# Optimization experiments

Hardware: AMD Instinct MI355X
Metric: run time of the kernel (lower is better)

## Reference

```python
import jax, jax.numpy as jnp
import numpy as np

DIM = 2048
NUM_HEADS = 16
HEAD_DIM = DIM // NUM_HEADS
ROPE_BASE = 10000.0


def _rotate_half(t):
    t1, t2 = jnp.split(t, 2, axis=-1)
    return jnp.concatenate([-t2, t1], axis=-1)


def _rope_sin_cos(seq_len):
    # fp32 angles, matching RoPE1D
    inv_freq = 1.0 / (ROPE_BASE ** (jnp.arange(0, HEAD_DIM, 2, dtype=jnp.float32) / HEAD_DIM))
    freqs = jnp.arange(seq_len, dtype=jnp.float32)[:, None] * inv_freq[None, :]  # [S, hd/2]
    angles = jnp.concatenate([freqs, freqs], axis=-1)  # [S, hd]
    return jnp.sin(angles), jnp.cos(angles)


def setup_inputs() -> dict:
    key = jax.random.key(0)
    ks = jax.random.split(key, 5)
    B, S = 2, 2048
    x = jax.random.normal(ks[0], (B, S, DIM), dtype=jnp.float32)
    scale = 1.0 / np.sqrt(DIM)
    W_qkv = jax.random.normal(ks[1], (DIM, 3 * DIM), dtype=jnp.float32) * scale
    b_qkv = jnp.zeros((3 * DIM,), dtype=jnp.float32)
    W_proj = jax.random.normal(ks[2], (DIM, DIM), dtype=jnp.float32) * scale
    b_proj = jnp.zeros((DIM,), dtype=jnp.float32)
    return {"x": x, "W_qkv": W_qkv, "b_qkv": b_qkv, "W_proj": W_proj, "b_proj": b_proj}


def reference(x, W_qkv, b_qkv, W_proj, b_proj):
    B, S, D = x.shape
    H, hd = NUM_HEADS, HEAD_DIM
    qkv = x @ W_qkv + b_qkv  # [B, S, 3D]
    qkv = qkv.reshape(B, S, 3, H, hd)
    q, k, v = qkv[:, :, 0], qkv[:, :, 1], qkv[:, :, 2]  # [B, S, H, hd]
    q, k, v = (t.transpose(0, 2, 1, 3) for t in (q, k, v))  # [B, H, S, hd]
    sin, cos = _rope_sin_cos(S)  # [S, hd]
    sin = sin[None, None]
    cos = cos[None, None]
    q = q * cos + _rotate_half(q) * sin
    k = k * cos + _rotate_half(k) * sin
    # scaled dot-product attention (non-causal, no mask, no dropout)
    scale = 1.0 / np.sqrt(hd).astype(np.float32)
    scores = jnp.einsum("bhqd,bhkd->bhqk", q, k) * scale
    attn = jax.nn.softmax(scores, axis=-1)
    out = jnp.einsum("bhqk,bhkd->bhqd", attn, v)  # [B, H, S, hd]
    out = out.transpose(0, 2, 1, 3).reshape(B, S, D)
    return out @ W_proj + b_proj
```

## Files before the change

### kernel.cpp

```cpp
#include <hip/hip_runtime.h>


typedef __attribute__((ext_vector_type(4))) float  f32x4;
typedef __attribute__((ext_vector_type(8))) short  short8;
typedef __attribute__((ext_vector_type(4))) float  fv4;
typedef __attribute__((ext_vector_type(4))) unsigned short us4;

#define MFMA16(accv, av, bv) \
  asm volatile("v_mfma_f32_16x16x32_bf16 %0, %1, %2, %0" : "+v"(accv) : "v"(av), "v"(bv))

__device__ __forceinline__ unsigned short f2bf(float f) {
  unsigned int u = __float_as_uint(f);
  u += 0x7fffu + ((u >> 16) & 1u);
  return (unsigned short)(u >> 16);
}

__device__ __forceinline__ void gl_lds16(const void* g, void* l) {
  __builtin_amdgcn_global_load_lds((const __attribute__((address_space(1))) void*)g,
                                   (__attribute__((address_space(3))) void*)l, 16, 0, 0);
}

__global__ void cvt_f32_bf16(const float* __restrict__ in,
                             unsigned short* __restrict__ out, int n4) {
  int i = blockIdx.x * blockDim.x + threadIdx.x;
  int stride = gridDim.x * blockDim.x;
  for (; i < n4; i += stride) {
    fv4 v = ((const fv4*)in)[i];
    us4 o;
    o[0] = f2bf(v[0]); o[1] = f2bf(v[1]); o[2] = f2bf(v[2]); o[3] = f2bf(v[3]);
    ((us4*)out)[i] = o;
  }
}

__global__ void transpose_cvt(const float* __restrict__ in,
                              unsigned short* __restrict__ out, int R, int C) {
  __shared__ float tile[32][33];
  int c0 = blockIdx.x * 32, r0 = blockIdx.y * 32;
  int tx = threadIdx.x, ty = threadIdx.y;
#pragma unroll
  for (int i = 0; i < 4; i++)
    tile[ty + i * 8][tx] = in[(size_t)(r0 + ty + i * 8) * C + c0 + tx];
  __syncthreads();
#pragma unroll
  for (int i = 0; i < 4; i++)
    out[(size_t)(c0 + ty + i * 8) * R + r0 + tx] = f2bf(tile[tx][ty + i * 8]);
}

__global__ __launch_bounds__(256, 2) void qkv_gemm(
    const unsigned short* __restrict__ A,
    const unsigned short* __restrict__ Bt,
    const float* __restrict__ bias,
    unsigned short* __restrict__ Qo,
    unsigned short* __restrict__ Ko,
    unsigned short* __restrict__ Vo)
{
  __shared__ __align__(16) unsigned short Al[128 * 64];
  __shared__ __align__(16) unsigned short Bl[128 * 64];

  const int NBX = 48, NWG = 1536;
  int bid = blockIdx.x;
  int nid = (bid & 7) * (NWG / 8) + (bid >> 3);
  int by = nid / NBX, bx = nid - by * NBX;

  int tid = threadIdx.x;
  int wv = tid >> 6, lane = tid & 63;
  int wr = wv >> 1, wc = wv & 1;
  int g = lane >> 4, c = lane & 15;

  int m0 = by * 128, n0 = bx * 128;

  f32x4 acc[4][4];
#pragma unroll
  for (int m = 0; m < 4; m++)
#pragma unroll
    for (int n = 0; n < 4; n++)
#pragma unroll
      for (int r = 0; r < 4; r++) acc[m][n][r] = 0.f;

  for (int k0 = 0; k0 < 2048; k0 += 64) {
#pragma unroll
    for (int i = 0; i < 4; i++) {
      int s = wv * 256 + i * 64 + lane;
      int row = s >> 3;
      int cb = (s & 7) ^ (row & 7);
      gl_lds16(A  + (size_t)(m0 + row) * 2048 + k0 + cb * 8,
               Al + (size_t)(wv * 256 + i * 64) * 8);
      gl_lds16(Bt + (size_t)(n0 + row) * 2048 + k0 + cb * 8,
               Bl + (size_t)(wv * 256 + i * 64) * 8);
    }
    __syncthreads();

    short8 af[4][2], bf[4][2];
#pragma unroll
    for (int m = 0; m < 4; m++) {
      int row = wr * 64 + m * 16 + c;
#pragma unroll
      for (int kc = 0; kc < 2; kc++)
        af[m][kc] = *(const short8*)(Al + row * 64 + (((kc * 4 + g) ^ (row & 7)) * 8));
    }
#pragma unroll
    for (int n = 0; n < 4; n++) {
      int gt = 2 * wc + (n & 1) + (n >> 1) * 4;
      int row = gt * 16 + c;
#pragma unroll
      for (int kc = 0; kc < 2; kc++)
        bf[n][kc] = *(const short8*)(Bl + row * 64 + (((kc * 4 + g) ^ (row & 7)) * 8));
    }
#pragma unroll
    for (int m = 0; m < 4; m++)
#pragma unroll
      for (int n = 0; n < 4; n++) {
        MFMA16(acc[m][n], af[m][0], bf[n][0]);
        MFMA16(acc[m][n], af[m][1], bf[n][1]);
      }
    __syncthreads();
  }

  int sel = bx >> 4;
  int h = bx & 15;
  int b = by >> 4;

  int dloc[4];
  float biasv[4];
#pragma unroll
  for (int n = 0; n < 4; n++) {
    int gt = 2 * wc + (n & 1) + (n >> 1) * 4;
    dloc[n] = gt * 16 + c;
    biasv[n] = bias[n0 + dloc[n]];
  }

  if (sel == 2) {
    unsigned short* Vs = Al;
    for (int p = 0; p < 2; p++) {
      if (wr == p) {
#pragma unroll
        for (int m = 0; m < 4; m++)
#pragma unroll
          for (int n = 0; n < 4; n++) {
            int d = dloc[n];
#pragma unroll
            for (int r = 0; r < 4; r++) {
              int srel = m * 16 + 4 * g + r;
              Vs[d * 64 + (srel ^ ((d & 7) << 3))] = f2bf(acc[m][n][r] + biasv[n]);
            }
          }
      }
      __syncthreads();
#pragma unroll
      for (int i = 0; i < 4; i++) {
        int seg = i * 256 + tid;
        int d = seg >> 3, slot = seg & 7;
        short8 val = *(const short8*)(Vs + d * 64 + ((slot ^ (d & 7)) * 8));
        int s_seq = (by & 15) * 128 + p * 64 + slot * 8;
        *(short8*)(Vo + ((size_t)((b * 16 + h) * 128 + d)) * 2048 + s_seq) = val;
      }
      __syncthreads();
    }
  } else {
    unsigned short* outp = (sel == 0) ? Qo : Ko;
    float qscale = (sel == 0) ? (0.08838834764831845f * 1.44269504088896340736f) : 1.0f;
    float invf[2];
#pragma unroll
    for (int j = 0; j < 2; j++)
      invf[j] = __expf(-(float)dloc[j] * 0.14391156831212787f);
    int srow_base = (by & 15) * 128 + wr * 64;
#pragma unroll
    for (int m = 0; m < 4; m++) {
#pragma unroll
      for (int j = 0; j < 2; j++) {
        int dlo = dloc[j];
#pragma unroll
        for (int r = 0; r < 4; r++) {
          int s_seq = srow_base + m * 16 + 4 * g + r;
          float ang = (float)s_seq * invf[j];
          float sn, cs;
          __sincosf(ang, &sn, &cs);
          float vlo = acc[m][j][r]     + biasv[j];
          float vhi = acc[m][j + 2][r] + biasv[j + 2];
          float rlo = (vlo * cs - vhi * sn) * qscale;
          float rhi = (vhi * cs + vlo * sn) * qscale;
          size_t base = ((size_t)((b * 16 + h) * 2048 + s_seq)) * 128;
          outp[base + dlo]      = f2bf(rlo);
          outp[base + dlo + 64] = f2bf(rhi);
        }
      }
    }
  }
}

__global__ __launch_bounds__(256, 2) void attn_kernel(
    const unsigned short* __restrict__ Qi,
    const unsigned short* __restrict__ Ki,
    const unsigned short* __restrict__ Vi,
    unsigned short* __restrict__ X2)
{
  __shared__ __align__(16) unsigned short Kl[2][64 * 128];
  __shared__ __align__(16) unsigned short Vl[2][128 * 64];
  __shared__ __align__(16) unsigned short Pl[4][32 * 64];

  int bid = blockIdx.x;
  int nid = (bid & 7) * 64 + (bid >> 3);
  int bh = nid >> 4, qblk = nid & 15;
  int tid = threadIdx.x, wv = tid >> 6, lane = tid & 63;
  int g = lane >> 4, c = lane & 15;

  const unsigned short* Kg = Ki + (size_t)bh * 2048 * 128;
  const unsigned short* Vg = Vi + (size_t)bh * 128 * 2048;
  const unsigned short* Qb = Qi + ((size_t)bh * 2048 + qblk * 128 + wv * 32) * 128;

  short8 qf[2][4];
#pragma unroll
  for (int qt = 0; qt < 2; qt++)
#pragma unroll
    for (int dc = 0; dc < 4; dc++)
      qf[qt][dc] = *(const short8*)(Qb + (size_t)(qt * 16 + c) * 128 + dc * 32 + g * 8);

  f32x4 accO[2][8];
#pragma unroll
  for (int qt = 0; qt < 2; qt++)
#pragma unroll
    for (int nt = 0; nt < 8; nt++)
#pragma unroll
      for (int r = 0; r < 4; r++) accO[qt][nt][r] = 0.f;
  float m_run[2] = {-3.0e38f, -3.0e38f};
  float l_run[2] = {0.f, 0.f};

  auto stage = [&](int bsel, int t0) {
#pragma unroll
    for (int j = 0; j < 4; j++) {
      int e = j * 256 + tid;
      int s = e >> 4, sl = e & 15;
      gl_lds16(Kg + (size_t)(t0 + s) * 128 + ((sl ^ (s & 7)) * 8),
               &Kl[bsel][(size_t)(j * 256 + wv * 64) * 8]);
    }
#pragma unroll
    for (int j = 0; j < 4; j++) {
      int e = j * 256 + tid;
      int d = e >> 3, sl = e & 7;
      gl_lds16(Vg + (size_t)d * 2048 + t0 + ((sl ^ (d & 7)) * 8),
               &Vl[bsel][(size_t)(j * 256 + wv * 64) * 8]);
    }
  };

  stage(0, 0);
  __syncthreads();

  int cur = 0;
  for (int t = 0; t < 32; t++) {
    if (t < 31) stage(cur ^ 1, (t + 1) * 64);

    const unsigned short* Kt_ = &Kl[cur][0];
    const unsigned short* Vt_ = &Vl[cur][0];
    unsigned short* Pw = &Pl[wv][0];

    f32x4 sc[2][4];
#pragma unroll
    for (int qt = 0; qt < 2; qt++)
#pragma unroll
      for (int kt = 0; kt < 4; kt++)
#pragma unroll
        for (int r = 0; r < 4; r++) sc[qt][kt][r] = 0.f;

#pragma unroll
    for (int kt = 0; kt < 4; kt++) {
      short8 kf[4];
#pragma unroll
      for (int dc = 0; dc < 4; dc++)
        kf[dc] = *(const short8*)(Kt_ + (size_t)(kt * 16 + c) * 128 +
                                  (((dc * 4 + g) ^ (c & 7)) * 8));
      __builtin_amdgcn_s_setprio(1);
#pragma unroll
      for (int dc = 0; dc < 4; dc++) {
        MFMA16(sc[0][kt], kf[dc], qf[0][dc]);
        MFMA16(sc[1][kt], kf[dc], qf[1][dc]);
      }
      __builtin_amdgcn_s_setprio(0);
    }

    float mx[2];
#pragma unroll
    for (int qt = 0; qt < 2; qt++) {
      f32x4 mv = sc[qt][0];
#pragma unroll
      for (int kt = 1; kt < 4; kt++)
#pragma unroll
        for (int r = 0; r < 4; r++) mv[r] = fmaxf(mv[r], sc[qt][kt][r]);
      float m0 = fmaxf(fmaxf(mv[0], mv[1]), fmaxf(mv[2], mv[3]));
      m0 = fmaxf(m0, __shfl_xor(m0, 16));
      m0 = fmaxf(m0, __shfl_xor(m0, 32));
      mx[qt] = m0;
    }
    if (__any((mx[0] > m_run[0]) || (mx[1] > m_run[1]))) {
#pragma unroll
      for (int qt = 0; qt < 2; qt++) {
        float mnew = fmaxf(m_run[qt], mx[qt]);
        float al = __builtin_exp2f(m_run[qt] - mnew);
        l_run[qt] *= al;
        m_run[qt] = mnew;
#pragma unroll
        for (int r = 0; r < 4; r++) {
          float alr = __shfl(al, 4 * g + r);
#pragma unroll
          for (int nt = 0; nt < 8; nt++) accO[qt][nt][r] *= alr;
        }
      }
    }
#pragma unroll
    for (int qt = 0; qt < 2; qt++) {
      float rs = 0.f;
#pragma unroll
      for (int kt = 0; kt < 4; kt++) {
        float p0 = __builtin_exp2f(sc[qt][kt][0] - m_run[qt]);
        float p1 = __builtin_exp2f(sc[qt][kt][1] - m_run[qt]);
        float p2 = __builtin_exp2f(sc[qt][kt][2] - m_run[qt]);
        float p3 = __builtin_exp2f(sc[qt][kt][3] - m_run[qt]);
        rs += (p0 + p1) + (p2 + p3);
        unsigned int lo, hi;
        asm("v_cvt_pk_bf16_f32 %0, %1, %2" : "=v"(lo) : "v"(p0), "v"(p1));
        asm("v_cvt_pk_bf16_f32 %0, %1, %2" : "=v"(hi) : "v"(p2), "v"(p3));
        uint2 pk; pk.x = lo; pk.y = hi;
        *(uint2*)(Pw + (size_t)(qt * 16 + c) * 64 +
                  (((kt * 2 + (g >> 1)) ^ (c & 7)) * 8) + (g & 1) * 4) = pk;
      }
      rs += __shfl_xor(rs, 16);
      rs += __shfl_xor(rs, 32);
      l_run[qt] += rs;
    }

    short8 pa[2][2];
#pragma unroll
    for (int qt = 0; qt < 2; qt++)
#pragma unroll
      for (int kc = 0; kc < 2; kc++)
        pa[qt][kc] = *(const short8*)(Pw + (size_t)(qt * 16 + c) * 64 +
                                      (((kc * 4 + g) ^ (c & 7)) * 8));
#pragma unroll
    for (int nt = 0; nt < 8; nt++) {
      short8 vf0 = *(const short8*)(Vt_ + (size_t)(nt * 16 + c) * 64 +
                                    ((g ^ (c & 7)) * 8));
      short8 vf1 = *(const short8*)(Vt_ + (size_t)(nt * 16 + c) * 64 +
                                    (((4 + g) ^ (c & 7)) * 8));
      __builtin_amdgcn_s_setprio(1);
      MFMA16(accO[0][nt], pa[0][0], vf0);
      MFMA16(accO[1][nt], pa[1][0], vf0);
      MFMA16(accO[0][nt], pa[0][1], vf1);
      MFMA16(accO[1][nt], pa[1][1], vf1);
      __builtin_amdgcn_s_setprio(0);
    }

    __syncthreads();
    cur ^= 1;
  }

  float rl[2] = {1.f / l_run[0], 1.f / l_run[1]};
  int b = bh >> 4, h = bh & 15;
  size_t rowbase = (size_t)b * 2048 + qblk * 128 + wv * 32;
#pragma unroll
  for (int qt = 0; qt < 2; qt++)
#pragma unroll
    for (int r = 0; r < 4; r++) {
      float rr = __shfl(rl[qt], 4 * g + r);
      size_t row = rowbase + qt * 16 + 4 * g + r;
#pragma unroll
      for (int nt = 0; nt < 8; nt++)
        X2[row * 2048 + h * 128 + nt * 16 + c] = f2bf(accO[qt][nt][r] * rr);
    }
}

__global__ __launch_bounds__(256, 2) void proj_gemm(
    const unsigned short* __restrict__ A,
    const unsigned short* __restrict__ Bt,
    const float* __restrict__ bias,
    float* __restrict__ Co)
{
  __shared__ __align__(16) unsigned short Al[128 * 64];
  __shared__ __align__(16) unsigned short Bl[128 * 64];

  const int NBX = 16, NWG = 512;
  int bid = blockIdx.x;
  int nid = (bid & 7) * (NWG / 8) + (bid >> 3);
  int by = nid / NBX, bx = nid - by * NBX;

  int tid = threadIdx.x;
  int wv = tid >> 6, lane = tid & 63;
  int wr = wv >> 1, wc = wv & 1;
  int g = lane >> 4, c = lane & 15;

  int m0 = by * 128, n0 = bx * 128;

  f32x4 acc[4][4];
#pragma unroll
  for (int m = 0; m < 4; m++)
#pragma unroll
    for (int n = 0; n < 4; n++)
#pragma unroll
      for (int r = 0; r < 4; r++) acc[m][n][r] = 0.f;

  for (int k0 = 0; k0 < 2048; k0 += 64) {
#pragma unroll
    for (int i = 0; i < 4; i++) {
      int s = wv * 256 + i * 64 + lane;
      int row = s >> 3;
      int cb = (s & 7) ^ (row & 7);
      gl_lds16(A  + (size_t)(m0 + row) * 2048 + k0 + cb * 8,
               Al + (size_t)(wv * 256 + i * 64) * 8);
      gl_lds16(Bt + (size_t)(n0 + row) * 2048 + k0 + cb * 8,
               Bl + (size_t)(wv * 256 + i * 64) * 8);
    }
    __syncthreads();

    short8 af[4][2], bf[4][2];
#pragma unroll
    for (int m = 0; m < 4; m++) {
      int row = wr * 64 + m * 16 + c;
#pragma unroll
      for (int kc = 0; kc < 2; kc++)
        af[m][kc] = *(const short8*)(Al + row * 64 + (((kc * 4 + g) ^ (row & 7)) * 8));
    }
#pragma unroll
    for (int n = 0; n < 4; n++) {
      int row = wc * 64 + n * 16 + c;
#pragma unroll
      for (int kc = 0; kc < 2; kc++)
        bf[n][kc] = *(const short8*)(Bl + row * 64 + (((kc * 4 + g) ^ (row & 7)) * 8));
    }
#pragma unroll
    for (int m = 0; m < 4; m++)
#pragma unroll
      for (int n = 0; n < 4; n++) {
        MFMA16(acc[m][n], af[m][0], bf[n][0]);
        MFMA16(acc[m][n], af[m][1], bf[n][1]);
      }
    __syncthreads();
  }

#pragma unroll
  for (int m = 0; m < 4; m++)
#pragma unroll
    for (int n = 0; n < 4; n++)
#pragma unroll
      for (int r = 0; r < 4; r++) {
        int row = m0 + wr * 64 + m * 16 + 4 * g + r;
        int col = n0 + wc * 64 + n * 16 + c;
        Co[(size_t)row * 2048 + col] = acc[m][n][r] + bias[col];
      }
}

extern "C" void kernel_launch(void* const* d_in, const int* in_sizes, int n_in,
                              void* d_out, int out_size, void* d_ws, size_t ws_size,
                              hipStream_t stream) {
  (void)in_sizes; (void)n_in; (void)out_size; (void)ws_size;

  const float* x      = (const float*)d_in[0];
  const float* W_qkv  = (const float*)d_in[1];
  const float* b_qkv  = (const float*)d_in[2];
  const float* W_proj = (const float*)d_in[3];
  const float* b_proj = (const float*)d_in[4];
  float* out = (float*)d_out;

  unsigned short* xb     = (unsigned short*)d_ws;
  unsigned short* wqkvT  = xb     + 8388608;
  unsigned short* wprojT = wqkvT  + 12582912;
  unsigned short* Qb     = wprojT + 4194304;
  unsigned short* Kb     = Qb     + 8388608;
  unsigned short* Vtb    = Kb     + 8388608;
  unsigned short* x2     = Vtb    + 8388608;

  cvt_f32_bf16<<<2048, 256, 0, stream>>>(x, xb, 8388608 / 4);
  transpose_cvt<<<dim3(192, 64), dim3(32, 8), 0, stream>>>(W_qkv, wqkvT, 2048, 6144);
  transpose_cvt<<<dim3(64, 64),  dim3(32, 8), 0, stream>>>(W_proj, wprojT, 2048, 2048);
  qkv_gemm<<<1536, 256, 0, stream>>>(xb, wqkvT, b_qkv, Qb, Kb, Vtb);
  attn_kernel<<<512, 256, 0, stream>>>(Qb, Kb, Vtb, x2);
  proj_gemm<<<512, 256, 0, stream>>>(x2, wprojT, b_proj, out);
}
```

Baseline: 397.6 us.

## Enlarge GEMM tiles and add 4-stage async LDS pipeline with waitcnt-based sync

```diff
diff --git a/kernel.cpp b/kernel.cpp
--- a/kernel.cpp
+++ b/kernel.cpp
@@ -46,7 +46,7 @@
     out[(size_t)(c0 + ty + i * 8) * R + r0 + tx] = f2bf(tile[tx][ty + i * 8]);
 }
 
-__global__ __launch_bounds__(256, 2) void qkv_gemm(
+__global__ __launch_bounds__(512, 2) void qkv_gemm(
     const unsigned short* __restrict__ A,
     const unsigned short* __restrict__ Bt,
     const float* __restrict__ bias,
@@ -54,124 +54,130 @@
     unsigned short* __restrict__ Ko,
     unsigned short* __restrict__ Vo)
 {
-  __shared__ __align__(16) unsigned short Al[128 * 64];
-  __shared__ __align__(16) unsigned short Bl[128 * 64];
-
-  const int NBX = 48, NWG = 1536;
+  __shared__ __align__(16) unsigned short SH[65536];
+
+  const int NWG = 384;
   int bid = blockIdx.x;
   int nid = (bid & 7) * (NWG / 8) + (bid >> 3);
-  int by = nid / NBX, bx = nid - by * NBX;
+  int by = nid / 24, bx = nid - by * 24;
 
   int tid = threadIdx.x;
   int wv = tid >> 6, lane = tid & 63;
-  int wr = wv >> 1, wc = wv & 1;
+  int wr = wv >> 2, wc = wv & 3;
   int g = lane >> 4, c = lane & 15;
 
-  int m0 = by * 128, n0 = bx * 128;
-
-  f32x4 acc[4][4];
-#pragma unroll
-  for (int m = 0; m < 4; m++)
+  int m0 = by * 256, n0 = bx * 256;
+
+  int lh = wc >> 1, jj = wc & 1;
+  int F[4];
+#pragma unroll
+  for (int n = 0; n < 4; n++) F[n] = 8 * lh + 2 * jj + (n & 1) + ((n >> 1) << 2);
+
+  f32x4 acc[8][4];
+#pragma unroll
+  for (int m = 0; m < 8; m++)
 #pragma unroll
     for (int n = 0; n < 4; n++)
 #pragma unroll
       for (int r = 0; r < 4; r++) acc[m][n][r] = 0.f;
 
-  for (int k0 = 0; k0 < 2048; k0 += 64) {
-#pragma unroll
-    for (int i = 0; i < 4; i++) {
-      int s = wv * 256 + i * 64 + lane;
-      int row = s >> 3;
-      int cb = (s & 7) ^ (row & 7);
-      gl_lds16(A  + (size_t)(m0 + row) * 2048 + k0 + cb * 8,
-               Al + (size_t)(wv * 256 + i * 64) * 8);
-      gl_lds16(Bt + (size_t)(n0 + row) * 2048 + k0 + cb * 8,
-               Bl + (size_t)(wv * 256 + i * 64) * 8);
-    }
+  auto stage = [&](int buf, int kt) {
+    int k0 = kt * 32;
+    unsigned short* Ad = SH + buf * 8192;
+    unsigned short* Bd = SH + 32768 + buf * 8192;
+#pragma unroll
+    for (int p = 0; p < 2; p++) {
+      int e = p * 512 + tid;
+      int row = e >> 2, sl = (e & 3) ^ ((row >> 1) & 3);
+      gl_lds16(A  + (size_t)(m0 + row) * 2048 + k0 + sl * 8,
+               Ad + p * 4096 + wv * 512);
+      gl_lds16(Bt + (size_t)(n0 + row) * 2048 + k0 + sl * 8,
+               Bd + p * 4096 + wv * 512);
+    }
+  };
+
+  stage(0, 0); stage(1, 1); stage(2, 2);
+
+  for (int t = 0; t < 64; t++) {
+    if (t < 62)       asm volatile("s_waitcnt vmcnt(8)" ::: "memory");
+    else if (t == 62) asm volatile("s_waitcnt vmcnt(4)" ::: "memory");
+    else              asm volatile("s_waitcnt vmcnt(0)" ::: "memory");
+    __builtin_amdgcn_s_barrier();
+
+    const unsigned short* Ab = SH + (t & 3) * 8192;
+    const unsigned short* Bb = SH + 32768 + (t & 3) * 8192;
+
+    short8 af[8], bfv[4];
+#pragma unroll
+    for (int m = 0; m < 8; m++) {
+      int row = wr * 128 + m * 16 + c;
+      af[m] = *(const short8*)(Ab + row * 32 + ((g ^ ((row >> 1) & 3)) << 3));
+    }
+#pragma unroll
+    for (int n = 0; n < 4; n++) {
+      int row = F[n] * 16 + c;
+      bfv[n] = *(const short8*)(Bb + row * 32 + ((g ^ ((row >> 1) & 3)) << 3));
+    }
+
+    if (t < 61) stage((t + 3) & 3, t + 3);
+
+    __builtin_amdgcn_s_setprio(1);
+#pragma unroll
+    for (int m = 0; m < 8; m++)
+#pragma unroll
+      for (int n = 0; n < 4; n++)
+        MFMA16(acc[m][n], af[m], bfv[n]);
+    __builtin_amdgcn_s_setprio(0);
+  }
+
+  int sel = bx >> 3;
+  int bxl = bx & 7;
+  int b = by >> 3;
+
+  float biasv[4];
+#pragma unroll
+  for (int n = 0; n < 4; n++) biasv[n] = bias[n0 + F[n] * 16 + c];
+
+  if (sel == 2) {
     __syncthreads();
-
-    short8 af[4][2], bf[4][2];
-#pragma unroll
-    for (int m = 0; m < 4; m++) {
-      int row = wr * 64 + m * 16 + c;
-#pragma unroll
-      for (int kc = 0; kc < 2; kc++)
-        af[m][kc] = *(const short8*)(Al + row * 64 + (((kc * 4 + g) ^ (row & 7)) * 8));
-    }
-#pragma unroll
-    for (int n = 0; n < 4; n++) {
-      int gt = 2 * wc + (n & 1) + (n >> 1) * 4;
-      int row = gt * 16 + c;
-#pragma unroll
-      for (int kc = 0; kc < 2; kc++)
-        bf[n][kc] = *(const short8*)(Bl + row * 64 + (((kc * 4 + g) ^ (row & 7)) * 8));
-    }
-#pragma unroll
-    for (int m = 0; m < 4; m++)
+    unsigned short* Vs = SH;
+#pragma unroll
+    for (int m = 0; m < 8; m++)
 #pragma unroll
       for (int n = 0; n < 4; n++) {
-        MFMA16(acc[m][n], af[m][0], bf[n][0]);
-        MFMA16(acc[m][n], af[m][1], bf[n][1]);
+        int dp = F[n] * 16 + c;
+        int sb = wr * 128 + m * 16 + 4 * g;
+        us4 pk;
+#pragma unroll
+        for (int r = 0; r < 4; r++) pk[r] = f2bf(acc[m][n][r] + biasv[n]);
+        *(us4*)(Vs + dp * 256 + (sb ^ ((dp & 7) << 3))) = pk;
       }
     __syncthreads();
-  }
-
-  int sel = bx >> 4;
-  int h = bx & 15;
-  int b = by >> 4;
-
-  int dloc[4];
-  float biasv[4];
-#pragma unroll
-  for (int n = 0; n < 4; n++) {
-    int gt = 2 * wc + (n & 1) + (n >> 1) * 4;
-    dloc[n] = gt * 16 + c;
-    biasv[n] = bias[n0 + dloc[n]];
-  }
-
-  if (sel == 2) {
-    unsigned short* Vs = Al;
-    for (int p = 0; p < 2; p++) {
-      if (wr == p) {
-#pragma unroll
-        for (int m = 0; m < 4; m++)
-#pragma unroll
-          for (int n = 0; n < 4; n++) {
-            int d = dloc[n];
-#pragma unroll
-            for (int r = 0; r < 4; r++) {
-              int srel = m * 16 + 4 * g + r;
-              Vs[d * 64 + (srel ^ ((d & 7) << 3))] = f2bf(acc[m][n][r] + biasv[n]);
-            }
-          }
-      }
-      __syncthreads();
-#pragma unroll
-      for (int i = 0; i < 4; i++) {
-        int seg = i * 256 + tid;
-        int d = seg >> 3, slot = seg & 7;
-        short8 val = *(const short8*)(Vs + d * 64 + ((slot ^ (d & 7)) * 8));
-        int s_seq = (by & 15) * 128 + p * 64 + slot * 8;
-        *(short8*)(Vo + ((size_t)((b * 16 + h) * 128 + d)) * 2048 + s_seq) = val;
-      }
-      __syncthreads();
+#pragma unroll
+    for (int it = 0; it < 16; it++) {
+      int u = it * 512 + tid;
+      int dp = u >> 5, ch = u & 31;
+      short8 val = *(const short8*)(Vs + dp * 256 + ((ch ^ (dp & 7)) << 3));
+      int head = bxl * 2 + (dp >> 7), d = dp & 127;
+      int sg = (by & 7) * 256 + ch * 8;
+      *(short8*)(Vo + ((size_t)((b * 16 + head) * 128 + d)) * 2048 + sg) = val;
     }
   } else {
     unsigned short* outp = (sel == 0) ? Qo : Ko;
     float qscale = (sel == 0) ? (0.08838834764831845f * 1.44269504088896340736f) : 1.0f;
+    int head = bxl * 2 + lh;
     float invf[2];
 #pragma unroll
     for (int j = 0; j < 2; j++)
-      invf[j] = __expf(-(float)dloc[j] * 0.14391156831212787f);
-    int srow_base = (by & 15) * 128 + wr * 64;
-#pragma unroll
-    for (int m = 0; m < 4; m++) {
+      invf[j] = __expf(-(float)((2 * jj + j) * 16 + c) * 0.14391156831212787f);
+#pragma unroll
+    for (int m = 0; m < 8; m++) {
 #pragma unroll
       for (int j = 0; j < 2; j++) {
-        int dlo = dloc[j];
+        int dlo = (2 * jj + j) * 16 + c;
 #pragma unroll
         for (int r = 0; r < 4; r++) {
-          int s_seq = srow_base + m * 16 + 4 * g + r;
+          int s_seq = (by & 7) * 256 + wr * 128 + m * 16 + 4 * g + r;
           float ang = (float)s_seq * invf[j];
           float sn, cs;
           __sincosf(ang, &sn, &cs);
@@ -179,7 +185,7 @@
           float vhi = acc[m][j + 2][r] + biasv[j + 2];
           float rlo = (vlo * cs - vhi * sn) * qscale;
           float rhi = (vhi * cs + vlo * sn) * qscale;
-          size_t base = ((size_t)((b * 16 + h) * 2048 + s_seq)) * 128;
+          size_t base = ((size_t)((b * 16 + head) * 2048 + s_seq)) * 128;
           outp[base + dlo]      = f2bf(rlo);
           outp[base + dlo + 64] = f2bf(rhi);
         }
@@ -367,26 +373,24 @@
     }
 }
 
-__global__ __launch_bounds__(256, 2) void proj_gemm(
+__global__ __launch_bounds__(512, 2) void proj_gemm(
     const unsigned short* __restrict__ A,
     const unsigned short* __restrict__ Bt,
     const float* __restrict__ bias,
     float* __restrict__ Co)
 {
-  __shared__ __align__(16) unsigned short Al[128 * 64];
-  __shared__ __align__(16) unsigned short Bl[128 * 64];
-
-  const int NBX = 16, NWG = 512;
+  __shared__ __align__(16) unsigned short SH[49152];
+
   int bid = blockIdx.x;
-  int nid = (bid & 7) * (NWG / 8) + (bid >> 3);
-  int by = nid / NBX, bx = nid - by * NBX;
+  int nid = (bid & 7) * 32 + (bid >> 3);
+  int by = nid >> 4, bx = nid & 15;
 
   int tid = threadIdx.x;
   int wv = tid >> 6, lane = tid & 63;
   int wr = wv >> 1, wc = wv & 1;
   int g = lane >> 4, c = lane & 15;
 
-  int m0 = by * 128, n0 = bx * 128;
+  int m0 = by * 256, n0 = bx * 128;
 
   f32x4 acc[4][4];
 #pragma unroll
@@ -396,42 +400,57 @@
 #pragma unroll
       for (int r = 0; r < 4; r++) acc[m][n][r] = 0.f;
 
-  for (int k0 = 0; k0 < 2048; k0 += 64) {
-#pragma unroll
-    for (int i = 0; i < 4; i++) {
-      int s = wv * 256 + i * 64 + lane;
-      int row = s >> 3;
-      int cb = (s & 7) ^ (row & 7);
-      gl_lds16(A  + (size_t)(m0 + row) * 2048 + k0 + cb * 8,
-               Al + (size_t)(wv * 256 + i * 64) * 8);
-      gl_lds16(Bt + (size_t)(n0 + row) * 2048 + k0 + cb * 8,
-               Bl + (size_t)(wv * 256 + i * 64) * 8);
-    }
-    __syncthreads();
-
-    short8 af[4][2], bf[4][2];
+  auto stage = [&](int buf, int kt) {
+    int k0 = kt * 32;
+    unsigned short* Ad = SH + buf * 8192;
+    unsigned short* Bd = SH + 32768 + buf * 4096;
+#pragma unroll
+    for (int p = 0; p < 2; p++) {
+      int e = p * 512 + tid;
+      int row = e >> 2, sl = (e & 3) ^ ((row >> 1) & 3);
+      gl_lds16(A + (size_t)(m0 + row) * 2048 + k0 + sl * 8,
+               Ad + p * 4096 + wv * 512);
+    }
+    {
+      int e = tid;
+      int row = e >> 2, sl = (e & 3) ^ ((row >> 1) & 3);
+      gl_lds16(Bt + (size_t)(n0 + row) * 2048 + k0 + sl * 8,
+               Bd + wv * 512);
+    }
+  };
+
+  stage(0, 0); stage(1, 1); stage(2, 2);
+
+  for (int t = 0; t < 64; t++) {
+    if (t < 62)       asm volatile("s_waitcnt vmcnt(6)" ::: "memory");
+    else if (t == 62) asm volatile("s_waitcnt vmcnt(3)" ::: "memory");
+    else              asm volatile("s_waitcnt vmcnt(0)" ::: "memory");
+    __builtin_amdgcn_s_barrier();
+
+    const unsigned short* Ab = SH + (t & 3) * 8192;
+    const unsigned short* Bb = SH + 32768 + (t & 3) * 4096;
+
+    short8 af[4], bfv[4];
 #pragma unroll
     for (int m = 0; m < 4; m++) {
       int row = wr * 64 + m * 16 + c;
-#pragma unroll
-      for (int kc = 0; kc < 2; kc++)
-        af[m][kc] = *(const short8*)(Al + row * 64 + (((kc * 4 + g) ^ (row & 7)) * 8));
+      af[m] = *(const short8*)(Ab + row * 32 + ((g ^ ((row >> 1) & 3)) << 3));
     }
 #pragma unroll
     for (int n = 0; n < 4; n++) {
-      int row = wc * 64 + n * 16 + c;
-#pragma unroll
-      for (int kc = 0; kc < 2; kc++)
-        bf[n][kc] = *(const short8*)(Bl + row * 64 + (((kc * 4 + g) ^ (row & 7)) * 8));
-    }
+      int row = (wc * 4 + n) * 16 + c;
+      bfv[n] = *(const short8*)(Bb + row * 32 + ((g ^ ((row >> 1) & 3)) << 3));
+    }
+
+    if (t < 61) stage((t + 3) & 3, t + 3);
+
+    __builtin_amdgcn_s_setprio(1);
 #pragma unroll
     for (int m = 0; m < 4; m++)
 #pragma unroll
-      for (int n = 0; n < 4; n++) {
-        MFMA16(acc[m][n], af[m][0], bf[n][0]);
-        MFMA16(acc[m][n], af[m][1], bf[n][1]);
-      }
-    __syncthreads();
+      for (int n = 0; n < 4; n++)
+        MFMA16(acc[m][n], af[m], bfv[n]);
+    __builtin_amdgcn_s_setprio(0);
   }
 
 #pragma unroll
@@ -469,7 +488,7 @@
   cvt_f32_bf16<<<2048, 256, 0, stream>>>(x, xb, 8388608 / 4);
   transpose_cvt<<<dim3(192, 64), dim3(32, 8), 0, stream>>>(W_qkv, wqkvT, 2048, 6144);
   transpose_cvt<<<dim3(64, 64),  dim3(32, 8), 0, stream>>>(W_proj, wprojT, 2048, 2048);
-  qkv_gemm<<<1536, 256, 0, stream>>>(xb, wqkvT, b_qkv, Qb, Kb, Vtb);
+  qkv_gemm<<<384, 512, 0, stream>>>(xb, wqkvT, b_qkv, Qb, Kb, Vtb);
   attn_kernel<<<512, 256, 0, stream>>>(Qb, Kb, Vtb, x2);
-  proj_gemm<<<512, 256, 0, stream>>>(x2, wprojT, b_proj, out);
-}
+  proj_gemm<<<256, 512, 0, stream>>>(x2, wprojT, b_proj, out);
+}
```

New measurement: 399.7 us. About the same (+0.5%).
